# Performance work log

Measured on AMD Instinct MI355X. Metric: run time of the kernel, lower is better.

## Reference

```python
import jax, jax.numpy as jnp
import numpy as np

H, N_PATCH, F, DIM = 12, 196, 8, 768
DH = DIM // H            # 64
D3 = 3 * DH              # per-head dim after 3*dim projection = 192
SCALE = float(np.sqrt(DH) * H)
B, S = 8, 1 + N_PATCH * F  # 1569


def setup_inputs() -> dict:
    key = jax.random.key(0)
    ks = jax.random.split(key, 12)
    w = lambda k, shp: (jax.random.normal(k, shp, dtype=jnp.float32) * 0.02)
    return {
        "x": jax.random.normal(ks[0], (B, S, DIM), dtype=jnp.float32),
        "Wq": w(ks[1], (DIM, 3 * DIM)), "bq": jnp.zeros((3 * DIM,), jnp.float32),
        "Wk": w(ks[2], (DIM, 3 * DIM)), "bk": jnp.zeros((3 * DIM,), jnp.float32),
        "Wv": w(ks[3], (DIM, 3 * DIM)), "bv": jnp.zeros((3 * DIM,), jnp.float32),
        "Wt": w(ks[4], (3 * DIM, DIM)), "bt": jnp.zeros((DIM,), jnp.float32),
        "Wf": w(ks[5], (3 * DIM, DIM)), "bf": jnp.zeros((DIM,), jnp.float32),
    }


def _heads(t):
    # [b, s, 3*dim] -> [b, H, s, D3]
    b, s, _ = t.shape
    return t.reshape(b, s, H, D3).transpose(0, 2, 1, 3)


def _merge(t):
    # [b, H, s, D3] -> [b, s, 3*dim]
    b, _, s, _ = t.shape
    return t.transpose(0, 2, 1, 3).reshape(b, s, H * D3)


def _attn(q, k, v):
    a = jax.nn.softmax(jnp.einsum('bhqd,bhkd->bhqk', q, k) / SCALE, axis=-1)
    return jnp.einsum('bhqk,bhkd->bhqd', a, v)


def reference(x, Wq, bq, Wk, bk, Wv, bv, Wt, bt, Wf, bf):
    patches = x[:, 1:, :]                       # [b, n*F, dim]
    # NOTE: faithful to original code: v_mat comes from self.k, k_mat from self.v
    qm = _heads(patches @ Wq + bq)
    vm = _heads(patches @ Wk + bk)
    km = _heads(patches @ Wv + bv)

    # CLS attention over full sequence (here v from self.v, k from self.k)
    q_cls = _heads(x[:, 0:1, :] @ Wq + bq)      # [b,H,1,D3]
    v_cls = _heads(x @ Wv + bv)
    k_cls = _heads(x @ Wk + bk)
    inter_cls = _attn(q_cls, k_cls, v_cls)      # [b,H,1,D3]

    # Stage 1: temporal attention per patch (patches 1..n-1), vectorized.
    # tokens are frame-major: index = frame*n + patch, so slice p::n == patch p across frames
    def per_patch(t):
        b = t.shape[0]
        return t.reshape(b, H, F, N_PATCH, D3)[:, :, :, 1:, :].transpose(0, 1, 3, 2, 4)  # [b,H,n-1,F,D3]
    q5, k5, v5 = per_patch(qm), per_patch(km), per_patch(vm)
    a1 = jax.nn.softmax(jnp.einsum('bhpfd,bhpgd->bhpfg', q5, k5) / SCALE, axis=-1)
    t1 = jnp.einsum('bhpfg,bhpgd->bhpfd', a1, v5).sum(axis=3)   # [b,H,n-1,D3]
    t1 = jnp.tile(t1, (1, 1, F, 1))                              # [b,H,(n-1)*F,D3]
    ti = _merge(t1) @ Wt + bt                                    # [b,(n-1)*F,dim]

    # Stage 2 (same qkv swap as stage 1)
    q2 = _heads(ti @ Wq + bq)
    v2 = _heads(ti @ Wk + bk)
    k2 = _heads(ti @ Wv + bv)
    outs = [_attn(q2[:, :, 0:N_PATCH], k2[:, :, 0:N_PATCH], v2[:, :, 0:N_PATCH]).sum(axis=2, keepdims=True)]
    for xi in range(1, F):  # small fixed loop over num_frames
        o = _attn(q2[:, :, xi:xi + N_PATCH], k2[:, :, xi::N_PATCH], v2[:, :, xi::N_PATCH])
        outs.append(o.sum(axis=2, keepdims=True))
    t2 = jnp.concatenate(outs, axis=2)                           # [b,H,F,D3]
    t2 = jnp.tile(t2, (1, 1, N_PATCH, 1))                        # [b,H,F*n,D3]

    full = jnp.concatenate([inter_cls, t2], axis=2)              # [b,H,1+n*F,D3]
    return _merge(full) @ Wf + bf                                # [b,S,dim]
```

## Files before the change

### kernel.cpp

```cpp
#include <hip/hip_runtime.h>
#include <math.h>

#define B_    8
#define SEQ   1569
#define DIMX  768
#define H_    12
#define D3    192
#define F_    8
#define NP    196
#define P1    195
#define NCOL  2304
#define RSCALE (1.0f/96.0f)
#define NCHUNK 16
#define CH     99
#define CLS_STRIDE 196

typedef __bf16 bf16_t;
typedef bf16_t bf16x8 __attribute__((ext_vector_type(8)));
typedef float  f32x4  __attribute__((ext_vector_type(4)));

__device__ __forceinline__ void load_lds16(const bf16_t* g, bf16_t* l) {
  __builtin_amdgcn_global_load_lds(
      (const __attribute__((address_space(1))) void*)g,
      (__attribute__((address_space(3))) void*)l, 16, 0, 0);
}

__device__ __forceinline__ float block_max256(float v, float* red) {
  #pragma unroll
  for (int o = 32; o > 0; o >>= 1) v = fmaxf(v, __shfl_xor(v, o, 64));
  __syncthreads();
  if ((threadIdx.x & 63) == 0) red[threadIdx.x >> 6] = v;
  __syncthreads();
  return fmaxf(fmaxf(red[0], red[1]), fmaxf(red[2], red[3]));
}

__device__ __forceinline__ float block_sum256(float v, float* red) {
  #pragma unroll
  for (int o = 32; o > 0; o >>= 1) v += __shfl_xor(v, o, 64);
  __syncthreads();
  if ((threadIdx.x & 63) == 0) red[threadIdx.x >> 6] = v;
  __syncthreads();
  return red[0] + red[1] + red[2] + red[3];
}

__global__ __launch_bounds__(256) void cast_f32_bf16(
    const float* __restrict__ in, bf16_t* __restrict__ out, int n4) {
  const int i = blockIdx.x * 256 + threadIdx.x;
  if (i >= n4) return;
  const float4 v = ((const float4*)in)[i];
  bf16_t o4[4] = {(bf16_t)v.x, (bf16_t)v.y, (bf16_t)v.z, (bf16_t)v.w};
  ((uint2*)out)[i] = *(uint2*)o4;
}

__global__ __launch_bounds__(256) void transpose_cast(
    const float* __restrict__ W, bf16_t* __restrict__ WT, int Kd, int Nd) {
  __shared__ float t[32][33];
  const int bn = blockIdx.x * 32;
  const int bk = blockIdx.y * 32;
  const int tx = threadIdx.x & 31, ty = threadIdx.x >> 5;
  #pragma unroll
  for (int i = 0; i < 32; i += 8)
    t[ty + i][tx] = W[(size_t)(bk + ty + i) * Nd + bn + tx];
  __syncthreads();
  #pragma unroll
  for (int i = 0; i < 32; i += 8)
    WT[(size_t)(bn + ty + i) * Kd + bk + tx] = (bf16_t)t[tx][ty + i];
}

__global__ __launch_bounds__(256) void gemm_mfma_bt(
    const bf16_t* __restrict__ A, const bf16_t* __restrict__ BT,
    const float* __restrict__ bias, void* __restrict__ C,
    int M, int N, int K, int outBf16) {
  __shared__ bf16_t As[128][32];
  __shared__ bf16_t Bs[128][32];
  const int tid  = threadIdx.x;
  const int wave = tid >> 6, lane = tid & 63;
  const int row0 = blockIdx.x * 128, col0 = blockIdx.y * 128;
  const int lrow = lane >> 2, lseg = lane & 3;

  int r0 = row0 + wave * 32 + lrow;
  int r1 = r0 + 16;
  if (r0 >= M) r0 = M - 1;
  if (r1 >= M) r1 = M - 1;
  const bf16_t* Ap0 = A + (size_t)r0 * K + lseg * 8;
  const bf16_t* Ap1 = A + (size_t)r1 * K + lseg * 8;
  const bf16_t* Bp0 = BT + (size_t)(col0 + wave * 32 + lrow) * K + lseg * 8;
  const bf16_t* Bp1 = Bp0 + (size_t)16 * K;
  bf16_t* lA0 = &As[wave * 32][0];
  bf16_t* lA1 = &As[wave * 32 + 16][0];
  bf16_t* lB0 = &Bs[wave * 32][0];
  bf16_t* lB1 = &Bs[wave * 32 + 16][0];

  const int m0 = (wave & 1) * 64, n0 = (wave >> 1) * 64;
  const int fr = lane & 15, k8 = (lane >> 4) * 8;
  f32x4 acc[4][4] = {};

  for (int k0 = 0; k0 < K; k0 += 32) {
    load_lds16(Ap0 + k0, lA0);
    load_lds16(Ap1 + k0, lA1);
    load_lds16(Bp0 + k0, lB0);
    load_lds16(Bp1 + k0, lB1);
    __syncthreads();

    bf16x8 af[4], bfr[4];
    #pragma unroll
    for (int i = 0; i < 4; ++i) {
      af[i]  = *(const bf16x8*)&As[m0 + i * 16 + fr][k8];
      bfr[i] = *(const bf16x8*)&Bs[n0 + i * 16 + fr][k8];
    }
    #pragma unroll
    for (int i = 0; i < 4; ++i)
      #pragma unroll
      for (int j = 0; j < 4; ++j)
        acc[i][j] = __builtin_amdgcn_mfma_f32_16x16x32_bf16(
            af[i], bfr[j], acc[i][j], 0, 0, 0);
    __syncthreads();
  }

  const int cc = lane & 15, cr4 = (lane >> 4) * 4;
  #pragma unroll
  for (int i = 0; i < 4; ++i) {
    #pragma unroll
    for (int j = 0; j < 4; ++j) {
      const int col = col0 + n0 + j * 16 + cc;
      const float bcol = bias[col];
      #pragma unroll
      for (int reg = 0; reg < 4; ++reg) {
        const int r = row0 + m0 + i * 16 + cr4 + reg;
        if (r < M) {
          const float v = acc[i][j][reg] + bcol;
          if (outBf16) ((bf16_t*)C)[(size_t)r * N + col] = (bf16_t)v;
          else         ((float*)C)[(size_t)r * N + col] = v;
        }
      }
    }
  }
}

__global__ __launch_bounds__(256) void xi0_scores_mfma(
    const bf16_t* __restrict__ Q2b, const bf16_t* __restrict__ K2b,
    float* __restrict__ Smat) {
  __shared__ bf16_t As[128][32];
  __shared__ bf16_t Bs[128][32];
  const int tid  = threadIdx.x;
  const int wave = tid >> 6, lane = tid & 63;
  const int row0 = blockIdx.x * 128, col0 = blockIdx.y * 128;
  const int bh = blockIdx.z;
  const int b = bh / H_, h = bh % H_;
  const bf16_t* Abase = Q2b + (size_t)b * P1 * NCOL + h * D3;
  const bf16_t* Bbase = K2b + (size_t)b * P1 * NCOL + h * D3;
  const int lrow = lane >> 2, lseg = lane & 3;

  int r0 = row0 + wave * 32 + lrow;
  int r1 = r0 + 16;
  if (r0 >= P1) r0 = P1 - 1;
  if (r1 >= P1) r1 = P1 - 1;
  int c0 = col0 + wave * 32 + lrow;
  int c1 = c0 + 16;
  if (c0 >= P1) c0 = P1 - 1;
  if (c1 >= P1) c1 = P1 - 1;
  const bf16_t* Ap0 = Abase + (size_t)r0 * NCOL + lseg * 8;
  const bf16_t* Ap1 = Abase + (size_t)r1 * NCOL + lseg * 8;
  const bf16_t* Bp0 = Bbase + (size_t)c0 * NCOL + lseg * 8;
  const bf16_t* Bp1 = Bbase + (size_t)c1 * NCOL + lseg * 8;
  bf16_t* lA0 = &As[wave * 32][0];
  bf16_t* lA1 = &As[wave * 32 + 16][0];
  bf16_t* lB0 = &Bs[wave * 32][0];
  bf16_t* lB1 = &Bs[wave * 32 + 16][0];

  const int m0 = (wave & 1) * 64, n0 = (wave >> 1) * 64;
  const int fr = lane & 15, k8 = (lane >> 4) * 8;
  f32x4 acc[4][4] = {};

  for (int k0 = 0; k0 < D3; k0 += 32) {
    load_lds16(Ap0 + k0, lA0);
    load_lds16(Ap1 + k0, lA1);
    load_lds16(Bp0 + k0, lB0);
    load_lds16(Bp1 + k0, lB1);
    __syncthreads();
    bf16x8 af[4], bfr[4];
    #pragma unroll
    for (int i = 0; i < 4; ++i) {
      af[i]  = *(const bf16x8*)&As[m0 + i * 16 + fr][k8];
      bfr[i] = *(const bf16x8*)&Bs[n0 + i * 16 + fr][k8];
    }
    #pragma unroll
    for (int i = 0; i < 4; ++i)
      #pragma unroll
      for (int j = 0; j < 4; ++j)
        acc[i][j] = __builtin_amdgcn_mfma_f32_16x16x32_bf16(
            af[i], bfr[j], acc[i][j], 0, 0, 0);
    __syncthreads();
  }

  float* S = Smat + (size_t)bh * P1 * P1;
  const int cc = lane & 15, cr4 = (lane >> 4) * 4;
  #pragma unroll
  for (int i = 0; i < 4; ++i)
    #pragma unroll
    for (int j = 0; j < 4; ++j) {
      const int col = col0 + n0 + j * 16 + cc;
      #pragma unroll
      for (int reg = 0; reg < 4; ++reg) {
        const int r = row0 + m0 + i * 16 + cr4 + reg;
        if (r < P1 && col < P1) S[(size_t)r * P1 + col] = acc[i][j][reg] * RSCALE;
      }
    }
}

__global__ __launch_bounds__(256) void xi0_finish_kernel(
    const float* __restrict__ Smat, const float* __restrict__ V2U,
    bf16_t* __restrict__ FULL9b) {
  const int bh = blockIdx.x;
  const int b = bh / H_, h = bh % H_;
  __shared__ float mrow[P1], inv_l[P1], g[P1];
  const float* S = Smat + (size_t)bh * P1 * P1;
  const int tid = threadIdx.x;

  if (tid < P1) {
    float m = -1e30f;
    for (int k = 0; k < P1; ++k) m = fmaxf(m, S[(size_t)tid * P1 + k]);
    float l = 0.f;
    for (int k = 0; k < P1; ++k)
      l += expf(S[(size_t)tid * P1 + k] - m) * ((k == 0) ? 2.f : 1.f);
    mrow[tid] = m;
    inv_l[tid] = ((tid == 0) ? 2.f : 1.f) / l;
  }
  __syncthreads();
  if (tid < P1) {
    float s = 0.f;
    for (int r = 0; r < P1; ++r)
      s += expf(S[(size_t)r * P1 + tid] - mrow[r]) * inv_l[r];
    g[tid] = s * ((tid == 0) ? 2.f : 1.f);
  }
  __syncthreads();
  if (tid < D3) {
    float acc = 0.f;
    const float* vbase = V2U + (size_t)b * P1 * NCOL + h * D3 + tid;
    for (int k = 0; k < P1; ++k) acc = fmaf(g[k], vbase[(size_t)k * NCOL], acc);
    FULL9b[((size_t)b * 9 + 1) * NCOL + h * D3 + tid] = (bf16_t)acc;
  }
}

__global__ __launch_bounds__(256) void cls_part_kernel(
    const bf16_t* __restrict__ XQ, const bf16_t* __restrict__ XK,
    const bf16_t* __restrict__ XV, float* __restrict__ CLSP, int b0) {
  const int h  = blockIdx.x % H_;
  const int bl = blockIdx.x / H_;
  const int b  = b0 + bl;
  const int c  = blockIdx.y;
  const int t0 = c * CH;
  const int tend = (t0 + CH < SEQ) ? t0 + CH : SEQ;
  __shared__ float qs[D3];
  __shared__ float sc[CH];
  __shared__ float red[4];
  const int tid = threadIdx.x;

  const bf16_t* Qr = XQ + (size_t)bl * SEQ * NCOL + h * D3;
  if (tid < 24) {
    const bf16x8 q8 = *(const bf16x8*)(Qr + tid * 8);
    #pragma unroll
    for (int m2 = 0; m2 < 8; ++m2) qs[tid * 8 + m2] = (float)q8[m2];
  }
  __syncthreads();

  float lmax = -1e30f;
  for (int t = t0 + tid; t < tend; t += 256) {
    const bf16_t* kr = XK + ((size_t)bl * SEQ + t) * NCOL + h * D3;
    float acc = 0.f;
    #pragma unroll 3
    for (int d = 0; d < D3; d += 8) {
      const bf16x8 k8 = *(const bf16x8*)(kr + d);
      #pragma unroll
      for (int m2 = 0; m2 < 8; ++m2) acc = fmaf(qs[d + m2], (float)k8[m2], acc);
    }
    acc *= RSCALE;
    sc[t - t0] = acc;
    lmax = fmaxf(lmax, acc);
  }
  const float m = block_max256(lmax, red);
  float lsum = 0.f;
  for (int t = t0 + tid; t < tend; t += 256) {
    const float e = expf(sc[t - t0] - m);
    sc[t - t0] = e;
    lsum += e;
  }
  const float L = block_sum256(lsum, red);
  __syncthreads();

  float* P = CLSP + ((size_t)(b * H_ + h) * NCHUNK + c) * CLS_STRIDE;
  if (tid < D3) {
    float acc = 0.f;
    const bf16_t* vbase = XV + ((size_t)bl * SEQ + t0) * NCOL + h * D3 + tid;
    for (int t = t0; t < tend; ++t)
      acc = fmaf(sc[t - t0], (float)vbase[(size_t)(t - t0) * NCOL], acc);
    P[tid] = acc;
  }
  if (tid == 192) P[192] = m;
  if (tid == 193) P[193] = L;
}

__global__ __launch_bounds__(256) void cls_combine_kernel(
    const float* __restrict__ CLSP, bf16_t* __restrict__ FULL9b) {
  const int bh = blockIdx.x;
  const int tid = threadIdx.x;
  const float* P = CLSP + (size_t)bh * NCHUNK * CLS_STRIDE;

  float M = -1e30f;
  #pragma unroll
  for (int c = 0; c < NCHUNK; ++c) M = fmaxf(M, P[c * CLS_STRIDE + 192]);
  float L = 0.f;
  float w[NCHUNK];
  #pragma unroll
  for (int c = 0; c < NCHUNK; ++c) {
    w[c] = expf(P[c * CLS_STRIDE + 192] - M);
    L += P[c * CLS_STRIDE + 193] * w[c];
  }
  if (tid < D3) {
    float acc = 0.f;
    #pragma unroll
    for (int c = 0; c < NCHUNK; ++c)
      acc = fmaf(w[c], P[c * CLS_STRIDE + tid], acc);
    const int b = bh / H_, h = bh % H_;
    FULL9b[((size_t)b * 9 + 0) * NCOL + h * D3 + tid] = (bf16_t)(acc / L);
  }
}

__global__ __launch_bounds__(64) void temporal_kernel(
    const bf16_t* __restrict__ XQ, const bf16_t* __restrict__ XK,
    const bf16_t* __restrict__ XV, bf16_t* __restrict__ T1U, int b0) {
  const int id = blockIdx.x;
  const int pi = id % P1;
  const int h  = (id / P1) % H_;
  const int bl = id / (P1 * H_);
  const int b  = b0 + bl;
  __shared__ float qs[8][196], ks[8][196];
  const int tid = threadIdx.x;

  #pragma unroll
  for (int i = 0; i < 6; ++i) {
    const int idx = tid + 64 * i;
    const int arr = idx / 192;
    const int c = idx % 192;
    const int f = c / 24, d0 = (c % 24) * 8;
    const size_t base = ((size_t)bl * SEQ + (size_t)f * NP + pi + 2) * NCOL + h * D3 + d0;
    const bf16x8 v8 = arr ? *(const bf16x8*)(XV + base)
                          : *(const bf16x8*)(XQ + base);
    float* dst = arr ? &ks[f][d0] : &qs[f][d0];
    #pragma unroll
    for (int m2 = 0; m2 < 8; ++m2) dst[m2] = (float)v8[m2];
  }
  __syncthreads();

  const int f = tid >> 3, g = tid & 7;
  float s = 0.f;
  for (int d = 0; d < D3; d += 4) {
    const float4 a4 = *(const float4*)&qs[f][d];
    const float4 b4 = *(const float4*)&ks[g][d];
    s = fmaf(a4.x, b4.x, s); s = fmaf(a4.y, b4.y, s);
    s = fmaf(a4.z, b4.z, s); s = fmaf(a4.w, b4.w, s);
  }
  s *= RSCALE;

  float m = s;
  #pragma unroll
  for (int o = 1; o < 8; o <<= 1) m = fmaxf(m, __shfl_xor(m, o, 64));
  const float e = expf(s - m);
  float sum = e;
  #pragma unroll
  for (int o = 1; o < 8; o <<= 1) sum += __shfl_xor(sum, o, 64);
  float a = e / sum;
  #pragma unroll
  for (int o = 8; o < 64; o <<= 1) a += __shfl_xor(a, o, 64);
  float wg[8];
  #pragma unroll
  for (int gg = 0; gg < 8; ++gg) wg[gg] = __shfl(a, gg, 64);

  const size_t vrow = (size_t)bl * SEQ * NCOL + h * D3;
  #pragma unroll
  for (int i = 0; i < 3; ++i) {
    const int d = tid + 64 * i;
    float o = 0.f;
    #pragma unroll
    for (int gg = 0; gg < 8; ++gg) {
      const bf16_t vv = XK[vrow + ((size_t)gg * NP + pi + 2) * NCOL + d];
      o = fmaf(wg[gg], (float)vv, o);
    }
    T1U[((size_t)b * P1 + pi) * NCOL + h * D3 + d] = (bf16_t)o;
  }
}

__global__ __launch_bounds__(256) void stage2_xi_kernel(
    const bf16_t* __restrict__ Q2b, const bf16_t* __restrict__ K2b,
    const float* __restrict__ V2U, bf16_t* __restrict__ FULL9b) {
  const int xi = 1 + blockIdx.x % 7;
  const int h  = (blockIdx.x / 7) % H_;
  const int b  = blockIdx.x / (7 * H_);
  __shared__ float Ks[8][196], Vs[8][196], Qs[32][196];
  __shared__ float Pp[32][8];
  const int tid = threadIdx.x;

  for (int idx = tid; idx < 192; idx += 256) {
    const int k = idx / 24, d0 = (idx % 24) * 8;
    const bf16x8 v8 = *(const bf16x8*)(K2b + ((size_t)(b * P1 + xi + k)) * NCOL + h * D3 + d0);
    #pragma unroll
    for (int m2 = 0; m2 < 8; ++m2) Ks[k][d0 + m2] = (float)v8[m2];
  }
  for (int idx = tid; idx < 384; idx += 256) {
    const int k = idx / 48, d0 = (idx % 48) * 4;
    *(float4*)&Vs[k][d0] =
        *(const float4*)(V2U + ((size_t)(b * P1 + xi + k)) * NCOL + h * D3 + d0);
  }

  float acc = 0.f;
  for (int c = 0; c < 7; ++c) {
    __syncthreads();
    for (int idx = tid; idx < 768; idx += 256) {
      const int qr = idx / 24, d0 = (idx % 24) * 8;
      const int rq = c * 32 + qr;
      if (rq < P1) {
        const bf16x8 v8 = *(const bf16x8*)(Q2b + ((size_t)(b * P1 + rq)) * NCOL + h * D3 + d0);
        #pragma unroll
        for (int m2 = 0; m2 < 8; ++m2) Qs[qr][d0 + m2] = (float)v8[m2];
      } else {
        #pragma unroll
        for (int m2 = 0; m2 < 8; ++m2) Qs[qr][d0 + m2] = 0.f;
      }
    }
    __syncthreads();
    const int grp = tid >> 3, k = tid & 7;
    float dot = 0.f;
    for (int d = 0; d < D3; d += 4) {
      const float4 a4 = *(const float4*)&Qs[grp][d];
      const float4 b4 = *(const float4*)&Ks[k][d];
      dot = fmaf(a4.x, b4.x, dot); dot = fmaf(a4.y, b4.y, dot);
      dot = fmaf(a4.z, b4.z, dot); dot = fmaf(a4.w, b4.w, dot);
    }
    dot *= RSCALE;
    float m = dot;
    #pragma unroll
    for (int o = 1; o < 8; o <<= 1) m = fmaxf(m, __shfl_xor(m, o, 64));
    const float e = expf(dot - m);
    float s = e;
    #pragma unroll
    for (int o = 1; o < 8; o <<= 1) s += __shfl_xor(s, o, 64);
    Pp[grp][k] = e / s;
    __syncthreads();
    if (tid < D3) {
      #pragma unroll 4
      for (int g2 = 0; g2 < 32; ++g2) {
        const int rq2 = c * 32 + g2;
        if (rq2 < P1) {
          const float mult = (rq2 == xi) ? 2.f : 1.f;
          float o = 0.f;
          #pragma unroll
          for (int kk = 0; kk < 8; ++kk) o = fmaf(Pp[g2][kk], Vs[kk][tid], o);
          acc = fmaf(mult, o, acc);
        }
      }
    }
  }
  if (tid < D3)
    FULL9b[((size_t)b * 9 + 1 + xi) * NCOL + h * D3 + tid] = (bf16_t)acc;
}

__global__ __launch_bounds__(256) void bcast_kernel(
    const float* __restrict__ OUT9, float* __restrict__ out) {
  const int idx = blockIdx.x * 256 + threadIdx.x;
  const int total = B_ * SEQ * (DIMX / 4);
  if (idx >= total) return;
  const int d4 = idx % (DIMX / 4);
  const int bs = idx / (DIMX / 4);
  const int s = bs % SEQ;
  const int b = bs / SEQ;
  const int row = (s == 0) ? 0 : 1 + ((s - 1) & 7);
  ((float4*)out)[idx] = ((const float4*)OUT9)[(size_t)(b * 9 + row) * (DIMX / 4) + d4];
}

extern "C" void kernel_launch(void* const* d_in, const int* in_sizes, int n_in,
                              void* d_out, int out_size, void* d_ws, size_t ws_size,
                              hipStream_t stream) {
  const float* x  = (const float*)d_in[0];
  const float* Wq = (const float*)d_in[1];
  const float* bq = (const float*)d_in[2];
  const float* Wk = (const float*)d_in[3];
  const float* bk = (const float*)d_in[4];
  const float* Wv = (const float*)d_in[5];
  const float* bv = (const float*)d_in[6];
  const float* Wt = (const float*)d_in[7];
  const float* bt = (const float*)d_in[8];
  const float* Wf = (const float*)d_in[9];
  const float* bf = (const float*)d_in[10];
  float* out = (float*)d_out;
  (void)in_sizes; (void)n_in; (void)out_size;

  char* ws = (char*)d_ws;
  size_t off = 0;
  auto alloc_f32 = [&](size_t elems) {
    size_t a = (off + 63) & ~(size_t)63;
    off = a + elems * sizeof(float);
    return (float*)(ws + a);
  };
  auto alloc_bf16 = [&](size_t elems) {
    size_t a = (off + 63) & ~(size_t)63;
    off = a + elems * sizeof(bf16_t);
    return (bf16_t*)(ws + a);
  };

  bf16_t* T1Ub   = alloc_bf16((size_t)B_ * P1 * NCOL);
  bf16_t* TIUb   = alloc_bf16((size_t)B_ * P1 * DIMX);
  bf16_t* Q2b    = alloc_bf16((size_t)B_ * P1 * NCOL);
  bf16_t* K2b    = alloc_bf16((size_t)B_ * P1 * NCOL);
  float*  V2U    = alloc_f32((size_t)B_ * P1 * NCOL);
  bf16_t* FULL9b = alloc_bf16((size_t)B_ * 9 * NCOL);
  float*  OUT9   = alloc_f32((size_t)B_ * 9 * DIMX);
  float*  Smat   = alloc_f32((size_t)B_ * H_ * P1 * P1);
  float*  CLSP   = alloc_f32((size_t)B_ * H_ * NCHUNK * CLS_STRIDE);
  bf16_t* WqT    = alloc_bf16((size_t)NCOL * DIMX);
  bf16_t* WkT    = alloc_bf16((size_t)NCOL * DIMX);
  bf16_t* WvT    = alloc_bf16((size_t)NCOL * DIMX);
  bf16_t* WtT    = alloc_bf16((size_t)DIMX * NCOL);
  bf16_t* WfT    = alloc_bf16((size_t)DIMX * NCOL);

  const size_t remain = (ws_size > off) ? (ws_size - off) : 0;
  int Bc = 8;
  while (Bc > 1 &&
         (size_t)Bc * SEQ * (3 * NCOL + DIMX) * sizeof(bf16_t) + 512 > remain)
    Bc >>= 1;
  bf16_t* XQb = alloc_bf16((size_t)Bc * SEQ * NCOL);
  bf16_t* XKb = alloc_bf16((size_t)Bc * SEQ * NCOL);
  bf16_t* XVb = alloc_bf16((size_t)Bc * SEQ * NCOL);
  bf16_t* xb  = alloc_bf16((size_t)Bc * SEQ * DIMX);

  transpose_cast<<<dim3(NCOL / 32, DIMX / 32), 256, 0, stream>>>(Wq, WqT, DIMX, NCOL);
  transpose_cast<<<dim3(NCOL / 32, DIMX / 32), 256, 0, stream>>>(Wk, WkT, DIMX, NCOL);
  transpose_cast<<<dim3(NCOL / 32, DIMX / 32), 256, 0, stream>>>(Wv, WvT, DIMX, NCOL);
  transpose_cast<<<dim3(DIMX / 32, NCOL / 32), 256, 0, stream>>>(Wt, WtT, NCOL, DIMX);
  transpose_cast<<<dim3(DIMX / 32, NCOL / 32), 256, 0, stream>>>(Wf, WfT, NCOL, DIMX);

  for (int b0 = 0; b0 < B_; b0 += Bc) {
    const int Mrows = Bc * SEQ;
    const int n4 = Mrows * DIMX / 4;
    cast_f32_bf16<<<dim3((n4 + 255) / 256), 256, 0, stream>>>(
        x + (size_t)b0 * SEQ * DIMX, xb, n4);
    dim3 g1((Mrows + 127) / 128, NCOL / 128);
    gemm_mfma_bt<<<g1, 256, 0, stream>>>(xb, WqT, bq, XQb, Mrows, NCOL, DIMX, 1);
    gemm_mfma_bt<<<g1, 256, 0, stream>>>(xb, WkT, bk, XKb, Mrows, NCOL, DIMX, 1);
    gemm_mfma_bt<<<g1, 256, 0, stream>>>(xb, WvT, bv, XVb, Mrows, NCOL, DIMX, 1);
    cls_part_kernel<<<dim3(Bc * H_, NCHUNK), 256, 0, stream>>>(XQb, XKb, XVb, CLSP, b0);
    temporal_kernel<<<dim3(Bc * P1 * H_), 64, 0, stream>>>(XQb, XKb, XVb, T1Ub, b0);
  }
  cls_combine_kernel<<<dim3(B_ * H_), 256, 0, stream>>>(CLSP, FULL9b);

  {
    dim3 g((B_ * P1 + 127) / 128, DIMX / 128);
    gemm_mfma_bt<<<g, 256, 0, stream>>>(T1Ub, WtT, bt, TIUb, B_ * P1, DIMX, NCOL, 1);
  }
  {
    dim3 g((B_ * P1 + 127) / 128, NCOL / 128);
    gemm_mfma_bt<<<g, 256, 0, stream>>>(TIUb, WqT, bq, Q2b, B_ * P1, NCOL, DIMX, 1);
    gemm_mfma_bt<<<g, 256, 0, stream>>>(TIUb, WkT, bk, V2U, B_ * P1, NCOL, DIMX, 0);
    gemm_mfma_bt<<<g, 256, 0, stream>>>(TIUb, WvT, bv, K2b, B_ * P1, NCOL, DIMX, 1);
  }

  xi0_scores_mfma<<<dim3(2, 2, B_ * H_), 256, 0, stream>>>(Q2b, K2b, Smat);
  xi0_finish_kernel<<<dim3(B_ * H_), 256, 0, stream>>>(Smat, V2U, FULL9b);
  stage2_xi_kernel<<<dim3(B_ * H_ * 7), 256, 0, stream>>>(Q2b, K2b, V2U, FULL9b);

  {
    dim3 g((B_ * 9 + 127) / 128, DIMX / 128);
    gemm_mfma_bt<<<g, 256, 0, stream>>>(FULL9b, WfT, bf, OUT9, B_ * 9, DIMX, NCOL, 0);
  }

  {
    const int total4 = B_ * SEQ * (DIMX / 4);
    bcast_kernel<<<dim3((total4 + 255) / 256), 256, 0, stream>>>(OUT9, out);
  }
}
```

Before: 824.8 us.

## Fuse Q/K/V projections into one GEMM with grouped tile order and fragment-major LDS

Concatenates the transposed Q, K and V weights and their biases so each projection stage runs one wide GEMM (N=6912) instead of three launches. The A tile is loaded once per K step for all three outputs. The GEMM uses a 1-D grid with grouped-M tile swizzling to improve L2 reuse. The LDS layout becomes fragment-major so each lane reads contiguous 16 bytes. The stage-2 V buffer is now stored in bf16 rather than fp32, which cuts memory traffic but lowers the precision of the V values used in stage 2. All consumers are updated to the interleaved row stride.

```diff
diff --git a/kernel.cpp b/kernel.cpp
--- a/kernel.cpp
+++ b/kernel.cpp
@@ -10,6 +10,7 @@
 #define NP    196
 #define P1    195
 #define NCOL  2304
+#define NS    6912
 #define RSCALE (1.0f/96.0f)
 #define NCHUNK 16
 #define CH     99
@@ -52,6 +53,18 @@
   ((uint2*)out)[i] = *(uint2*)o4;
 }
 
+__global__ __launch_bounds__(256) void concat_bias_kernel(
+    const float* __restrict__ bq, const float* __restrict__ bk,
+    const float* __restrict__ bv, float* __restrict__ qkvb) {
+  const int i = blockIdx.x * 256 + threadIdx.x;
+  if (i >= NS) return;
+  float v;
+  if (i < NCOL) v = bq[i];
+  else if (i < 2 * NCOL) v = bk[i - NCOL];
+  else v = bv[i - 2 * NCOL];
+  qkvb[i] = v;
+}
+
 __global__ __launch_bounds__(256) void transpose_cast(
     const float* __restrict__ W, bf16_t* __restrict__ WT, int Kd, int Nd) {
   __shared__ float t[32][33];
@@ -70,29 +83,38 @@
 __global__ __launch_bounds__(256) void gemm_mfma_bt(
     const bf16_t* __restrict__ A, const bf16_t* __restrict__ BT,
     const float* __restrict__ bias, void* __restrict__ C,
-    int M, int N, int K, int outBf16) {
-  __shared__ bf16_t As[128][32];
-  __shared__ bf16_t Bs[128][32];
+    int M, int N, int K, int MT, int NT, int GROUPM, int outBf16) {
+  __shared__ bf16_t As[128 * 32];
+  __shared__ bf16_t Bs[128 * 32];
   const int tid  = threadIdx.x;
   const int wave = tid >> 6, lane = tid & 63;
-  const int row0 = blockIdx.x * 128, col0 = blockIdx.y * 128;
-  const int lrow = lane >> 2, lseg = lane & 3;
-
-  int r0 = row0 + wave * 32 + lrow;
-  int r1 = r0 + 16;
-  if (r0 >= M) r0 = M - 1;
-  if (r1 >= M) r1 = M - 1;
-  const bf16_t* Ap0 = A + (size_t)r0 * K + lseg * 8;
-  const bf16_t* Ap1 = A + (size_t)r1 * K + lseg * 8;
-  const bf16_t* Bp0 = BT + (size_t)(col0 + wave * 32 + lrow) * K + lseg * 8;
+
+  const int pid   = blockIdx.x;
+  const int npg   = GROUPM * NT;
+  const int group = pid / npg;
+  const int first_m = group * GROUPM;
+  int gsm = MT - first_m; if (gsm > GROUPM) gsm = GROUPM;
+  const int lpid  = pid % npg;
+  const int m_tile = first_m + lpid % gsm;
+  const int n_tile = lpid / gsm;
+  const int row0 = m_tile * 128, col0 = n_tile * 128;
+
+  const int fr = lane & 15, kg = lane >> 4;
+  int ra0 = row0 + wave * 32 + fr;
+  int ra1 = ra0 + 16;
+  if (ra0 >= M) ra0 = M - 1;
+  if (ra1 >= M) ra1 = M - 1;
+  const bf16_t* Ap0 = A + (size_t)ra0 * K + kg * 8;
+  const bf16_t* Ap1 = A + (size_t)ra1 * K + kg * 8;
+  const bf16_t* Bp0 = BT + (size_t)(col0 + wave * 32 + fr) * K + kg * 8;
   const bf16_t* Bp1 = Bp0 + (size_t)16 * K;
-  bf16_t* lA0 = &As[wave * 32][0];
-  bf16_t* lA1 = &As[wave * 32 + 16][0];
-  bf16_t* lB0 = &Bs[wave * 32][0];
-  bf16_t* lB1 = &Bs[wave * 32 + 16][0];
+  bf16_t* lA0 = &As[(wave * 2 + 0) * 512];
+  bf16_t* lA1 = &As[(wave * 2 + 1) * 512];
+  bf16_t* lB0 = &Bs[(wave * 2 + 0) * 512];
+  bf16_t* lB1 = &Bs[(wave * 2 + 1) * 512];
 
   const int m0 = (wave & 1) * 64, n0 = (wave >> 1) * 64;
-  const int fr = lane & 15, k8 = (lane >> 4) * 8;
+  const int mb = (wave & 1) * 4,  nb = (wave >> 1) * 4;
   f32x4 acc[4][4] = {};
 
   for (int k0 = 0; k0 < K; k0 += 32) {
@@ -105,8 +127,8 @@
     bf16x8 af[4], bfr[4];
     #pragma unroll
     for (int i = 0; i < 4; ++i) {
-      af[i]  = *(const bf16x8*)&As[m0 + i * 16 + fr][k8];
-      bfr[i] = *(const bf16x8*)&Bs[n0 + i * 16 + fr][k8];
+      af[i]  = *(const bf16x8*)&As[(mb + i) * 512 + lane * 8];
+      bfr[i] = *(const bf16x8*)&Bs[(nb + i) * 512 + lane * 8];
     }
     #pragma unroll
     for (int i = 0; i < 4; ++i)
@@ -138,38 +160,37 @@
 }
 
 __global__ __launch_bounds__(256) void xi0_scores_mfma(
-    const bf16_t* __restrict__ Q2b, const bf16_t* __restrict__ K2b,
-    float* __restrict__ Smat) {
-  __shared__ bf16_t As[128][32];
-  __shared__ bf16_t Bs[128][32];
+    const bf16_t* __restrict__ QKV2, float* __restrict__ Smat) {
+  __shared__ bf16_t As[128 * 32];
+  __shared__ bf16_t Bs[128 * 32];
   const int tid  = threadIdx.x;
   const int wave = tid >> 6, lane = tid & 63;
   const int row0 = blockIdx.x * 128, col0 = blockIdx.y * 128;
   const int bh = blockIdx.z;
   const int b = bh / H_, h = bh % H_;
-  const bf16_t* Abase = Q2b + (size_t)b * P1 * NCOL + h * D3;
-  const bf16_t* Bbase = K2b + (size_t)b * P1 * NCOL + h * D3;
-  const int lrow = lane >> 2, lseg = lane & 3;
-
-  int r0 = row0 + wave * 32 + lrow;
-  int r1 = r0 + 16;
-  if (r0 >= P1) r0 = P1 - 1;
-  if (r1 >= P1) r1 = P1 - 1;
-  int c0 = col0 + wave * 32 + lrow;
-  int c1 = c0 + 16;
-  if (c0 >= P1) c0 = P1 - 1;
-  if (c1 >= P1) c1 = P1 - 1;
-  const bf16_t* Ap0 = Abase + (size_t)r0 * NCOL + lseg * 8;
-  const bf16_t* Ap1 = Abase + (size_t)r1 * NCOL + lseg * 8;
-  const bf16_t* Bp0 = Bbase + (size_t)c0 * NCOL + lseg * 8;
-  const bf16_t* Bp1 = Bbase + (size_t)c1 * NCOL + lseg * 8;
-  bf16_t* lA0 = &As[wave * 32][0];
-  bf16_t* lA1 = &As[wave * 32 + 16][0];
-  bf16_t* lB0 = &Bs[wave * 32][0];
-  bf16_t* lB1 = &Bs[wave * 32 + 16][0];
+  const bf16_t* Abase = QKV2 + (size_t)b * P1 * NS + h * D3;
+  const bf16_t* Bbase = QKV2 + (size_t)b * P1 * NS + 2 * NCOL + h * D3;
+
+  const int fr = lane & 15, kg = lane >> 4;
+  int ra0 = row0 + wave * 32 + fr;
+  int ra1 = ra0 + 16;
+  if (ra0 >= P1) ra0 = P1 - 1;
+  if (ra1 >= P1) ra1 = P1 - 1;
+  int cb0 = col0 + wave * 32 + fr;
+  int cb1 = cb0 + 16;
+  if (cb0 >= P1) cb0 = P1 - 1;
+  if (cb1 >= P1) cb1 = P1 - 1;
+  const bf16_t* Ap0 = Abase + (size_t)ra0 * NS + kg * 8;
+  const bf16_t* Ap1 = Abase + (size_t)ra1 * NS + kg * 8;
+  const bf16_t* Bp0 = Bbase + (size_t)cb0 * NS + kg * 8;
+  const bf16_t* Bp1 = Bbase + (size_t)cb1 * NS + kg * 8;
+  bf16_t* lA0 = &As[(wave * 2 + 0) * 512];
+  bf16_t* lA1 = &As[(wave * 2 + 1) * 512];
+  bf16_t* lB0 = &Bs[(wave * 2 + 0) * 512];
+  bf16_t* lB1 = &Bs[(wave * 2 + 1) * 512];
 
   const int m0 = (wave & 1) * 64, n0 = (wave >> 1) * 64;
-  const int fr = lane & 15, k8 = (lane >> 4) * 8;
+  const int mb = (wave & 1) * 4,  nb = (wave >> 1) * 4;
   f32x4 acc[4][4] = {};
 
   for (int k0 = 0; k0 < D3; k0 += 32) {
@@ -181,8 +202,8 @@
     bf16x8 af[4], bfr[4];
     #pragma unroll
     for (int i = 0; i < 4; ++i) {
-      af[i]  = *(const bf16x8*)&As[m0 + i * 16 + fr][k8];
-      bfr[i] = *(const bf16x8*)&Bs[n0 + i * 16 + fr][k8];
+      af[i]  = *(const bf16x8*)&As[(mb + i) * 512 + lane * 8];
+      bfr[i] = *(const bf16x8*)&Bs[(nb + i) * 512 + lane * 8];
     }
     #pragma unroll
     for (int i = 0; i < 4; ++i)
@@ -209,7 +230,7 @@
 }
 
 __global__ __launch_bounds__(256) void xi0_finish_kernel(
-    const float* __restrict__ Smat, const float* __restrict__ V2U,
+    const float* __restrict__ Smat, const bf16_t* __restrict__ QKV2,
     bf16_t* __restrict__ FULL9b) {
   const int bh = blockIdx.x;
   const int b = bh / H_, h = bh % H_;
@@ -236,15 +257,15 @@
   __syncthreads();
   if (tid < D3) {
     float acc = 0.f;
-    const float* vbase = V2U + (size_t)b * P1 * NCOL + h * D3 + tid;
-    for (int k = 0; k < P1; ++k) acc = fmaf(g[k], vbase[(size_t)k * NCOL], acc);
+    const bf16_t* vbase = QKV2 + (size_t)b * P1 * NS + NCOL + h * D3 + tid;
+    for (int k = 0; k < P1; ++k)
+      acc = fmaf(g[k], (float)vbase[(size_t)k * NS], acc);
     FULL9b[((size_t)b * 9 + 1) * NCOL + h * D3 + tid] = (bf16_t)acc;
   }
 }
 
 __global__ __launch_bounds__(256) void cls_part_kernel(
-    const bf16_t* __restrict__ XQ, const bf16_t* __restrict__ XK,
-    const bf16_t* __restrict__ XV, float* __restrict__ CLSP, int b0) {
+    const bf16_t* __restrict__ XQKV, float* __restrict__ CLSP, int b0) {
   const int h  = blockIdx.x % H_;
   const int bl = blockIdx.x / H_;
   const int b  = b0 + bl;
@@ -256,7 +277,7 @@
   __shared__ float red[4];
   const int tid = threadIdx.x;
 
-  const bf16_t* Qr = XQ + (size_t)bl * SEQ * NCOL + h * D3;
+  const bf16_t* Qr = XQKV + (size_t)bl * SEQ * NS + h * D3;
   if (tid < 24) {
     const bf16x8 q8 = *(const bf16x8*)(Qr + tid * 8);
     #pragma unroll
@@ -266,7 +287,7 @@
 
   float lmax = -1e30f;
   for (int t = t0 + tid; t < tend; t += 256) {
-    const bf16_t* kr = XK + ((size_t)bl * SEQ + t) * NCOL + h * D3;
+    const bf16_t* kr = XQKV + ((size_t)bl * SEQ + t) * NS + NCOL + h * D3;
     float acc = 0.f;
     #pragma unroll 3
     for (int d = 0; d < D3; d += 8) {
@@ -291,9 +312,9 @@
   float* P = CLSP + ((size_t)(b * H_ + h) * NCHUNK + c) * CLS_STRIDE;
   if (tid < D3) {
     float acc = 0.f;
-    const bf16_t* vbase = XV + ((size_t)bl * SEQ + t0) * NCOL + h * D3 + tid;
+    const bf16_t* vbase = XQKV + ((size_t)bl * SEQ + t0) * NS + 2 * NCOL + h * D3 + tid;
     for (int t = t0; t < tend; ++t)
-      acc = fmaf(sc[t - t0], (float)vbase[(size_t)(t - t0) * NCOL], acc);
+      acc = fmaf(sc[t - t0], (float)vbase[(size_t)(t - t0) * NS], acc);
     P[tid] = acc;
   }
   if (tid == 192) P[192] = m;
@@ -327,8 +348,7 @@
 }
 
 __global__ __launch_bounds__(64) void temporal_kernel(
-    const bf16_t* __restrict__ XQ, const bf16_t* __restrict__ XK,
-    const bf16_t* __restrict__ XV, bf16_t* __restrict__ T1U, int b0) {
+    const bf16_t* __restrict__ XQKV, bf16_t* __restrict__ T1U, int b0) {
   const int id = blockIdx.x;
   const int pi = id % P1;
   const int h  = (id / P1) % H_;
@@ -343,9 +363,9 @@
     const int arr = idx / 192;
     const int c = idx % 192;
     const int f = c / 24, d0 = (c % 24) * 8;
-    const size_t base = ((size_t)bl * SEQ + (size_t)f * NP + pi + 2) * NCOL + h * D3 + d0;
-    const bf16x8 v8 = arr ? *(const bf16x8*)(XV + base)
-                          : *(const bf16x8*)(XQ + base);
+    const size_t base = ((size_t)bl * SEQ + (size_t)f * NP + pi + 2) * NS +
+                        (arr ? 2 * NCOL : 0) + h * D3 + d0;
+    const bf16x8 v8 = *(const bf16x8*)(XQKV + base);
     float* dst = arr ? &ks[f][d0] : &qs[f][d0];
     #pragma unroll
     for (int m2 = 0; m2 < 8; ++m2) dst[m2] = (float)v8[m2];
@@ -376,14 +396,14 @@
   #pragma unroll
   for (int gg = 0; gg < 8; ++gg) wg[gg] = __shfl(a, gg, 64);
 
-  const size_t vrow = (size_t)bl * SEQ * NCOL + h * D3;
+  const size_t vrow = (size_t)bl * SEQ * NS + NCOL + h * D3;
   #pragma unroll
   for (int i = 0; i < 3; ++i) {
     const int d = tid + 64 * i;
     float o = 0.f;
     #pragma unroll
     for (int gg = 0; gg < 8; ++gg) {
-      const bf16_t vv = XK[vrow + ((size_t)gg * NP + pi + 2) * NCOL + d];
+      const bf16_t vv = XQKV[vrow + ((size_t)gg * NP + pi + 2) * NS + d];
       o = fmaf(wg[gg], (float)vv, o);
     }
     T1U[((size_t)b * P1 + pi) * NCOL + h * D3 + d] = (bf16_t)o;
@@ -391,8 +411,7 @@
 }
 
 __global__ __launch_bounds__(256) void stage2_xi_kernel(
-    const bf16_t* __restrict__ Q2b, const bf16_t* __restrict__ K2b,
-    const float* __restrict__ V2U, bf16_t* __restrict__ FULL9b) {
+    const bf16_t* __restrict__ QKV2, bf16_t* __restrict__ FULL9b) {
   const int xi = 1 + blockIdx.x % 7;
   const int h  = (blockIdx.x / 7) % H_;
   const int b  = blockIdx.x / (7 * H_);
@@ -402,14 +421,17 @@
 
   for (int idx = tid; idx < 192; idx += 256) {
     const int k = idx / 24, d0 = (idx % 24) * 8;
-    const bf16x8 v8 = *(const bf16x8*)(K2b + ((size_t)(b * P1 + xi + k)) * NCOL + h * D3 + d0);
+    const bf16x8 v8 = *(const bf16x8*)(QKV2 + ((size_t)(b * P1 + xi + k)) * NS +
+                                       2 * NCOL + h * D3 + d0);
     #pragma unroll
     for (int m2 = 0; m2 < 8; ++m2) Ks[k][d0 + m2] = (float)v8[m2];
   }
-  for (int idx = tid; idx < 384; idx += 256) {
-    const int k = idx / 48, d0 = (idx % 48) * 4;
-    *(float4*)&Vs[k][d0] =
-        *(const float4*)(V2U + ((size_t)(b * P1 + xi + k)) * NCOL + h * D3 + d0);
+  for (int idx = tid; idx < 192; idx += 256) {
+    const int k = idx / 24, d0 = (idx % 24) * 8;
+    const bf16x8 v8 = *(const bf16x8*)(QKV2 + ((size_t)(b * P1 + xi + k)) * NS +
+                                       NCOL + h * D3 + d0);
+    #pragma unroll
+    for (int m2 = 0; m2 < 8; ++m2) Vs[k][d0 + m2] = (float)v8[m2];
   }
 
   float acc = 0.f;
@@ -419,7 +441,8 @@
       const int qr = idx / 24, d0 = (idx % 24) * 8;
       const int rq = c * 32 + qr;
       if (rq < P1) {
-        const bf16x8 v8 = *(const bf16x8*)(Q2b + ((size_t)(b * P1 + rq)) * NCOL + h * D3 + d0);
+        const bf16x8 v8 = *(const bf16x8*)(QKV2 + ((size_t)(b * P1 + rq)) * NS +
+                                           h * D3 + d0);
         #pragma unroll
         for (int m2 = 0; m2 < 8; ++m2) Qs[qr][d0 + m2] = (float)v8[m2];
       } else {
@@ -509,67 +532,66 @@
 
   bf16_t* T1Ub   = alloc_bf16((size_t)B_ * P1 * NCOL);
   bf16_t* TIUb   = alloc_bf16((size_t)B_ * P1 * DIMX);
-  bf16_t* Q2b    = alloc_bf16((size_t)B_ * P1 * NCOL);
-  bf16_t* K2b    = alloc_bf16((size_t)B_ * P1 * NCOL);
-  float*  V2U    = alloc_f32((size_t)B_ * P1 * NCOL);
+  bf16_t* QKV2b  = alloc_bf16((size_t)B_ * P1 * NS);
   bf16_t* FULL9b = alloc_bf16((size_t)B_ * 9 * NCOL);
   float*  OUT9   = alloc_f32((size_t)B_ * 9 * DIMX);
   float*  Smat   = alloc_f32((size_t)B_ * H_ * P1 * P1);
   float*  CLSP   = alloc_f32((size_t)B_ * H_ * NCHUNK * CLS_STRIDE);
-  bf16_t* WqT    = alloc_bf16((size_t)NCOL * DIMX);
-  bf16_t* WkT    = alloc_bf16((size_t)NCOL * DIMX);
-  bf16_t* WvT    = alloc_bf16((size_t)NCOL * DIMX);
+  float*  QKVbias= alloc_f32(NS);
+  bf16_t* WqkvT  = alloc_bf16((size_t)3 * NCOL * DIMX);
   bf16_t* WtT    = alloc_bf16((size_t)DIMX * NCOL);
   bf16_t* WfT    = alloc_bf16((size_t)DIMX * NCOL);
 
   const size_t remain = (ws_size > off) ? (ws_size - off) : 0;
   int Bc = 8;
   while (Bc > 1 &&
-         (size_t)Bc * SEQ * (3 * NCOL + DIMX) * sizeof(bf16_t) + 512 > remain)
+         (size_t)Bc * SEQ * (NS + DIMX) * sizeof(bf16_t) + 512 > remain)
     Bc >>= 1;
-  bf16_t* XQb = alloc_bf16((size_t)Bc * SEQ * NCOL);
-  bf16_t* XKb = alloc_bf16((size_t)Bc * SEQ * NCOL);
-  bf16_t* XVb = alloc_bf16((size_t)Bc * SEQ * NCOL);
-  bf16_t* xb  = alloc_bf16((size_t)Bc * SEQ * DIMX);
-
-  transpose_cast<<<dim3(NCOL / 32, DIMX / 32), 256, 0, stream>>>(Wq, WqT, DIMX, NCOL);
-  transpose_cast<<<dim3(NCOL / 32, DIMX / 32), 256, 0, stream>>>(Wk, WkT, DIMX, NCOL);
-  transpose_cast<<<dim3(NCOL / 32, DIMX / 32), 256, 0, stream>>>(Wv, WvT, DIMX, NCOL);
+  bf16_t* XQKVb = alloc_bf16((size_t)Bc * SEQ * NS);
+  bf16_t* xb    = alloc_bf16((size_t)Bc * SEQ * DIMX);
+
+  transpose_cast<<<dim3(NCOL / 32, DIMX / 32), 256, 0, stream>>>(
+      Wq, WqkvT + 0 * (size_t)NCOL * DIMX, DIMX, NCOL);
+  transpose_cast<<<dim3(NCOL / 32, DIMX / 32), 256, 0, stream>>>(
+      Wk, WqkvT + 1 * (size_t)NCOL * DIMX, DIMX, NCOL);
+  transpose_cast<<<dim3(NCOL / 32, DIMX / 32), 256, 0, stream>>>(
+      Wv, WqkvT + 2 * (size_t)NCOL * DIMX, DIMX, NCOL);
   transpose_cast<<<dim3(DIMX / 32, NCOL / 32), 256, 0, stream>>>(Wt, WtT, NCOL, DIMX);
   transpose_cast<<<dim3(DIMX / 32, NCOL / 32), 256, 0, stream>>>(Wf, WfT, NCOL, DIMX);
+  concat_bias_kernel<<<dim3((NS + 255) / 256), 256, 0, stream>>>(bq, bk, bv, QKVbias);
 
   for (int b0 = 0; b0 < B_; b0 += Bc) {
     const int Mrows = Bc * SEQ;
     const int n4 = Mrows * DIMX / 4;
     cast_f32_bf16<<<dim3((n4 + 255) / 256), 256, 0, stream>>>(
         x + (size_t)b0 * SEQ * DIMX, xb, n4);
-    dim3 g1((Mrows + 127) / 128, NCOL / 128);
-    gemm_mfma_bt<<<g1, 256, 0, stream>>>(xb, WqT, bq, XQb, Mrows, NCOL, DIMX, 1);
-    gemm_mfma_bt<<<g1, 256, 0, stream>>>(xb, WkT, bk, XKb, Mrows, NCOL, DIMX, 1);
-    gemm_mfma_bt<<<g1, 256, 0, stream>>>(xb, WvT, bv, XVb, Mrows, NCOL, DIMX, 1);
-    cls_part_kernel<<<dim3(Bc * H_, NCHUNK), 256, 0, stream>>>(XQb, XKb, XVb, CLSP, b0);
-    temporal_kernel<<<dim3(Bc * P1 * H_), 64, 0, stream>>>(XQb, XKb, XVb, T1Ub, b0);
+    const int MT = (Mrows + 127) / 128, NT = NS / 128;
+    gemm_mfma_bt<<<dim3(MT * NT), 256, 0, stream>>>(
+        xb, WqkvT, QKVbias, XQKVb, Mrows, NS, DIMX, MT, NT, 8, 1);
+    cls_part_kernel<<<dim3(Bc * H_, NCHUNK), 256, 0, stream>>>(XQKVb, CLSP, b0);
+    temporal_kernel<<<dim3(Bc * P1 * H_), 64, 0, stream>>>(XQKVb, T1Ub, b0);
   }
   cls_combine_kernel<<<dim3(B_ * H_), 256, 0, stream>>>(CLSP, FULL9b);
 
   {
-    dim3 g((B_ * P1 + 127) / 128, DIMX / 128);
-    gemm_mfma_bt<<<g, 256, 0, stream>>>(T1Ub, WtT, bt, TIUb, B_ * P1, DIMX, NCOL, 1);
+    const int MT = (B_ * P1 + 127) / 128, NT = DIMX / 128;
+    gemm_mfma_bt<<<dim3(MT * NT), 256, 0, stream>>>(
+        T1Ub, WtT, bt, TIUb, B_ * P1, DIMX, NCOL, MT, NT, 4, 1);
   }
   {
-    dim3 g((B_ * P1 + 127) / 128, NCOL / 128);
-    gemm_mfma_bt<<<g, 256, 0, stream>>>(TIUb, WqT, bq, Q2b, B_ * P1, NCOL, DIMX, 1);
-    gemm_mfma_bt<<<g, 256, 0, stream>>>(TIUb, WkT, bk, V2U, B_ * P1, NCOL, DIMX, 0);
-    gemm_mfma_bt<<<g, 256, 0, stream>>>(TIUb, WvT, bv, K2b, B_ * P1, NCOL, DIMX, 1);
-  }
-
-  xi0_scores_mfma<<<dim3(2, 2, B_ * H_), 256, 0, stream>>>(Q2b, K2b, Smat);
-  xi0_finish_kernel<<<dim3(B_ * H_), 256, 0, stream>>>(Smat, V2U, FULL9b);
-  stage2_xi_kernel<<<dim3(B_ * H_ * 7), 256, 0, stream>>>(Q2b, K2b, V2U, FULL9b);
+    const int MT = (B_ * P1 + 127) / 128, NT = NS / 128;
+    gemm_mfma_bt<<<dim3(MT * NT), 256, 0, stream>>>(
+        TIUb, WqkvT, QKVbias, QKV2b, B_ * P1, NS, DIMX, MT, NT, 4, 1);
+  }
+
+  xi0_scores_mfma<<<dim3(2, 2, B_ * H_), 256, 0, stream>>>(QKV2b, Smat);
+  xi0_finish_kernel<<<dim3(B_ * H_), 256, 0, stream>>>(Smat, QKV2b, FULL9b);
+  stage2_xi_kernel<<<dim3(B_ * H_ * 7), 256, 0, stream>>>(QKV2b, FULL9b);
 
   {
-    dim3 g((B_ * 9 + 127) / 128, DIMX / 128);
-    gemm_mfma_bt<<<g, 256, 0, stream>>>(FULL9b, WfT, bf, OUT9, B_ * 9, DIMX, NCOL, 0);
+    const int MT = 1, NT = DIMX / 128;
+    gemm_mfma_bt<<<dim3(MT * NT), 256, 0, stream>>>(
+        FULL9b, WfT, bf, OUT9, B_ * 9, DIMX, NCOL, MT, NT, 1, 0);
   }
 
   {
```

Measured after the change: 834.7 us. About the same (+1.2%).
